# Optimization experiments

Measured on AMD Instinct MI355X. Metric: run time of the kernel, lower is better.

The kernel has to match this reference:

```python
import jax, jax.numpy as jnp
import numpy as np

N = 131072
MUL = 128                      # multiplicity of each irrep block in the input
IN_DIM = MUL * (1 + 3 + 5)     # 128x0e + 128x1o + 128x2e = 1152
INV_SQRT_MUL = 1.0 / np.sqrt(MUL)  # e3nn o3.Linear path normalization (fan_in = 128)

# --- Clebsch-Gordan (wigner 3j) tensors for 1o x 1o -> 0e, 1e, 2e ------------
# e3nn real basis ordering for l=1 is (y, z, x): index 0=y, 1=z, 2=x.

def _w3j_110():
    # 0e output: dot product; sum of squares of entries = 1
    return np.eye(3, dtype=np.float32) / np.sqrt(3.0)

def _w3j_111():
    # 1e output: Levi-Civita (cross product), normalized so sum of squares = 1
    eps = np.zeros((3, 3, 3), np.float32)
    for i, j, k in [(0, 1, 2), (1, 2, 0), (2, 0, 1)]:
        eps[i, j, k] = 1.0
        eps[j, i, k] = -1.0
    return eps / np.sqrt(6.0)

def _w3j_112():
    # 2e output: symmetric traceless rank-2 part.
    # l=2 component order: (xy, yz, 3z^2-r^2, xz, x^2-y^2); l=1 axes (y,z,x).
    Y, Z, X = 0, 1, 2
    s2 = 1.0 / np.sqrt(2.0)
    s6 = 1.0 / np.sqrt(6.0)
    M = np.zeros((3, 3, 5), np.float32)
    M[X, Y, 0] = M[Y, X, 0] = s2
    M[Y, Z, 1] = M[Z, Y, 1] = s2
    M[X, X, 2] = -s6; M[Y, Y, 2] = -s6; M[Z, Z, 2] = 2.0 * s6
    M[X, Z, 3] = M[Z, X, 3] = s2
    M[X, X, 4] = s2; M[Y, Y, 4] = -s2
    return M / np.sqrt(5.0)

_C0 = jnp.asarray(_w3j_110())
_C1 = jnp.asarray(_w3j_111())
_C2 = jnp.asarray(_w3j_112())
# path weights sqrt(dim(irrep_out)) for irrep_normalization='component',
# path_normalization='element' with fan = mul1*mul2 = 1
_PW0 = 1.0
_PW1 = float(np.sqrt(3.0))
_PW2 = float(np.sqrt(5.0))


def setup_inputs() -> dict:
    key = jax.random.key(0)
    k1, k2, k3, k4 = jax.random.split(key, 4)
    x = jax.random.normal(k1, (N, IN_DIM), jnp.float32)
    W1 = jax.random.normal(k2, (MUL, MUL), jnp.float32)   # 128x1o -> 128x1o
    W2 = jax.random.normal(k3, (MUL, 2), jnp.float32)     # 128x1o -> 2x1o
    tp_w = jax.random.normal(k4, (3,), jnp.float32)       # one weight per CG path
    return {"x": x, "W1": W1, "W2": W2, "tp_w": tp_w}


def reference(x, W1, W2, tp_w):
    n = x.shape[0]
    # o3.Linear(128x0e+128x1o+128x2e -> 128x1o): only the 1o block connects.
    x1o = x[:, MUL:MUL + 3 * MUL].reshape(n, MUL, 3)
    y = jnp.einsum('nuc,uv->nvc', x1o, W1) * INV_SQRT_MUL   # [N,128,3]
    y = jax.nn.silu(y)                                      # elementwise, as in torch
    y = jnp.einsum('nuc,uv->nvc', y, W2) * INV_SQRT_MUL     # [N,2,3] == 2x1o
    a, b = y[:, 0], y[:, 1]                                 # split y[:, :3], y[:, 3:]
    out0 = (tp_w[0] * _PW0) * jnp.einsum('ij,ni,nj->n', _C0, a, b)[:, None]  # [N,1]
    out1 = (tp_w[1] * _PW1) * jnp.einsum('ijk,ni,nj->nk', _C1, a, b)          # [N,3]
    out2 = (tp_w[2] * _PW2) * jnp.einsum('ijk,ni,nj->nk', _C2, a, b)          # [N,5]
    return jnp.concatenate([out0, out1, out2], axis=-1)     # [N,9] (0e+1e+2e)
```

## Files before the change

kernel.cpp:

```cpp
#include <hip/hip_runtime.h>
#include <hip/hip_bf16.h>

#define MULC 128
#define IN_DIM 1152
#define ROWS_PER_WG 64
#define NTHREADS 256
#define W1T_PITCH 136

typedef __attribute__((ext_vector_type(8))) short bf16x8;
typedef __attribute__((ext_vector_type(4))) float f32x4;
typedef __attribute__((ext_vector_type(4))) unsigned short u16x4;

__device__ __forceinline__ unsigned short f2bf(float f) {
    unsigned int b = __builtin_bit_cast(unsigned int, f);
    b += 0x7fffu + ((b >> 16) & 1u);
    return (unsigned short)(b >> 16);
}

#define LOADC(r0,r1,r2,r3,r4,r5, kc) {                                  \
    const float4* p_ = (const float4*)(xbase + 96 * (kc));              \
    r0 = p_[0]; r1 = p_[1]; r2 = p_[2]; r3 = p_[3]; r4 = p_[4]; r5 = p_[5]; }

#define FRAGS(F0,F1,F2, r0,r1,r2,r3,r4,r5)                                         \
    bf16x8 F0 = { (short)f2bf(r0.x), (short)f2bf(r0.w), (short)f2bf(r1.z),         \
                  (short)f2bf(r2.y), (short)f2bf(r3.x), (short)f2bf(r3.w),         \
                  (short)f2bf(r4.z), (short)f2bf(r5.y) };                          \
    bf16x8 F1 = { (short)f2bf(r0.y), (short)f2bf(r1.x), (short)f2bf(r1.w),         \
                  (short)f2bf(r2.z), (short)f2bf(r3.y), (short)f2bf(r4.x),         \
                  (short)f2bf(r4.w), (short)f2bf(r5.z) };                          \
    bf16x8 F2 = { (short)f2bf(r0.z), (short)f2bf(r1.y), (short)f2bf(r2.x),         \
                  (short)f2bf(r2.w), (short)f2bf(r3.z), (short)f2bf(r4.y),         \
                  (short)f2bf(r5.x), (short)f2bf(r5.w) };

#define MFMA_STEP(kc, F0,F1,F2)                                                     \
    _Pragma("unroll")                                                               \
    for (int nt = 0; nt < 8; ++nt) {                                                \
        bf16x8 bfr = *(const bf16x8*)&lds[(nt * 16 + li) * W1T_PITCH + (kc) * 32 + g * 8]; \
        acc[0][nt] = __builtin_amdgcn_mfma_f32_16x16x32_bf16(F0, bfr, acc[0][nt], 0, 0, 0); \
        acc[1][nt] = __builtin_amdgcn_mfma_f32_16x16x32_bf16(F1, bfr, acc[1][nt], 0, 0, 0); \
        acc[2][nt] = __builtin_amdgcn_mfma_f32_16x16x32_bf16(F2, bfr, acc[2][nt], 0, 0, 0); \
    }

__global__ __launch_bounds__(NTHREADS, 2)
void nltp_kernel(const float* __restrict__ x, const float* __restrict__ W1,
                 const float* __restrict__ W2, const float* __restrict__ tpw,
                 float* __restrict__ out)
{
    __shared__ __align__(16) unsigned short lds[128 * W1T_PITCH];
    const int t  = threadIdx.x;
    const int n0 = blockIdx.x * ROWS_PER_WG;
    const int l  = t & 63;
    const int w  = t >> 6;
    const int g  = l >> 4;
    const int li = l & 15;

    const float* xbase = x + (size_t)(n0 + 16 * w + li) * IN_DIM + MULC + 24 * g;

    float4 a0,a1,a2,a3,a4,a5, b0,b1,b2,b3,b4,b5;
    LOADC(a0,a1,a2,a3,a4,a5, 0);

    for (int it = 0; it < 16; ++it) {
        int tau = it * 256 + t;
        int v   = tau & 127;
        int u   = (tau >> 7) * 4;
        float f0 = W1[(u + 0) * MULC + v];
        float f1 = W1[(u + 1) * MULC + v];
        float f2 = W1[(u + 2) * MULC + v];
        float f3 = W1[(u + 3) * MULC + v];
        u16x4 pk = { f2bf(f0), f2bf(f1), f2bf(f2), f2bf(f3) };
        *(u16x4*)&lds[v * W1T_PITCH + u] = pk;
    }
    __syncthreads();

    f32x4 acc[3][8];
#pragma unroll
    for (int c = 0; c < 3; ++c)
#pragma unroll
        for (int nt = 0; nt < 8; ++nt)
            acc[c][nt] = (f32x4){0.f, 0.f, 0.f, 0.f};

    LOADC(b0,b1,b2,b3,b4,b5, 1);
    { FRAGS(fa0,fa1,fa2, a0,a1,a2,a3,a4,a5); MFMA_STEP(0, fa0,fa1,fa2); }
    LOADC(a0,a1,a2,a3,a4,a5, 2);
    { FRAGS(fb0,fb1,fb2, b0,b1,b2,b3,b4,b5); MFMA_STEP(1, fb0,fb1,fb2); }
    LOADC(b0,b1,b2,b3,b4,b5, 3);
    { FRAGS(fc0,fc1,fc2, a0,a1,a2,a3,a4,a5); MFMA_STEP(2, fc0,fc1,fc2); }
    { FRAGS(fd0,fd1,fd2, b0,b1,b2,b3,b4,b5); MFMA_STEP(3, fd0,fd1,fd2); }

    const float inv = 0.08838834764831845f;
    float w2a[8], w2b[8];
#pragma unroll
    for (int nt = 0; nt < 8; ++nt) {
        float2 p = *(const float2*)(W2 + 2 * (nt * 16 + li));
        w2a[nt] = p.x; w2b[nt] = p.y;
    }
    float pa[3][4], pb[3][4];
#pragma unroll
    for (int c = 0; c < 3; ++c)
#pragma unroll
        for (int rg = 0; rg < 4; ++rg) { pa[c][rg] = 0.f; pb[c][rg] = 0.f; }

#pragma unroll
    for (int c = 0; c < 3; ++c)
#pragma unroll
        for (int nt = 0; nt < 8; ++nt)
#pragma unroll
            for (int rg = 0; rg < 4; ++rg) {
                float y = acc[c][nt][rg] * inv;
                float s = y / (1.f + __expf(-y));
                pa[c][rg] += s * w2a[nt];
                pb[c][rg] += s * w2b[nt];
            }

#pragma unroll
    for (int c = 0; c < 3; ++c)
#pragma unroll
        for (int rg = 0; rg < 4; ++rg) {
            float va = pa[c][rg], vb = pb[c][rg];
            va += __shfl_xor(va, 1, 16); vb += __shfl_xor(vb, 1, 16);
            va += __shfl_xor(va, 2, 16); vb += __shfl_xor(vb, 2, 16);
            va += __shfl_xor(va, 4, 16); vb += __shfl_xor(vb, 4, 16);
            va += __shfl_xor(va, 8, 16); vb += __shfl_xor(vb, 8, 16);
            pa[c][rg] = va * inv;
            pb[c][rg] = vb * inv;
        }

    const float tw0 = tpw[0], tw1 = tpw[1], tw2 = tpw[2];
    const float k0 = tw0 * 0.5773502691896258f;
    const float k1 = tw1 * 0.7071067811865476f;
    const float s2 = 0.7071067811865476f;
    const float s6 = 0.4082482904638631f;

#pragma unroll
    for (int rg = 0; rg < 4; ++rg) {
        float a_0 = pa[0][rg], a_1 = pa[1][rg], a_2 = pa[2][rg];
        float b_0 = pb[0][rg], b_1 = pb[1][rg], b_2 = pb[2][rg];
        float o0 = k0 * (a_0 * b_0 + a_1 * b_1 + a_2 * b_2);
        float o1 = k1 * (a_1 * b_2 - a_2 * b_1);
        float o2 = k1 * (a_2 * b_0 - a_0 * b_2);
        float o3 = k1 * (a_0 * b_1 - a_1 * b_0);
        float o4 = tw2 * (s2 * (a_2 * b_0 + a_0 * b_2));
        float o5 = tw2 * (s2 * (a_0 * b_1 + a_1 * b_0));
        float o6 = tw2 * (s6 * (2.f * a_1 * b_1 - a_2 * b_2 - a_0 * b_0));
        float o7 = tw2 * (s2 * (a_2 * b_1 + a_1 * b_2));
        float o8 = tw2 * (s2 * (a_2 * b_2 - a_0 * b_0));
        float o = li == 0 ? o0 : li == 1 ? o1 : li == 2 ? o2 : li == 3 ? o3 :
                  li == 4 ? o4 : li == 5 ? o5 : li == 6 ? o6 : li == 7 ? o7 : o8;
        if (li < 9) {
            int row = n0 + 16 * w + 4 * g + rg;
            out[row * 9 + li] = o;
        }
    }
}

extern "C" void kernel_launch(void* const* d_in, const int* in_sizes, int n_in,
                              void* d_out, int out_size, void* d_ws, size_t ws_size,
                              hipStream_t stream) {
    const float* x   = (const float*)d_in[0];
    const float* W1  = (const float*)d_in[1];
    const float* W2  = (const float*)d_in[2];
    const float* tpw = (const float*)d_in[3];
    float* out = (float*)d_out;
    const int n = in_sizes[0] / IN_DIM;
    dim3 grid(n / ROWS_PER_WG);
    nltp_kernel<<<grid, NTHREADS, 0, stream>>>(x, W1, W2, tpw, out);
}
```

Baseline: 64.73 us.

## Stage x tile through swizzled LDS with contiguous row loads

```diff
diff --git a/kernel.cpp b/kernel.cpp
--- a/kernel.cpp
+++ b/kernel.cpp
@@ -5,11 +5,12 @@
 #define IN_DIM 1152
 #define ROWS_PER_WG 64
 #define NTHREADS 256
-#define W1T_PITCH 136
 
 typedef __attribute__((ext_vector_type(8))) short bf16x8;
 typedef __attribute__((ext_vector_type(4))) float f32x4;
-typedef __attribute__((ext_vector_type(4))) unsigned short u16x4;
+
+#define A_BASE 16384
+#define A_PLANE 8192
 
 __device__ __forceinline__ unsigned short f2bf(float f) {
     unsigned int b = __builtin_bit_cast(unsigned int, f);
@@ -17,36 +18,12 @@
     return (unsigned short)(b >> 16);
 }
 
-#define LOADC(r0,r1,r2,r3,r4,r5, kc) {                                  \
-    const float4* p_ = (const float4*)(xbase + 96 * (kc));              \
-    r0 = p_[0]; r1 = p_[1]; r2 = p_[2]; r3 = p_[3]; r4 = p_[4]; r5 = p_[5]; }
-
-#define FRAGS(F0,F1,F2, r0,r1,r2,r3,r4,r5)                                         \
-    bf16x8 F0 = { (short)f2bf(r0.x), (short)f2bf(r0.w), (short)f2bf(r1.z),         \
-                  (short)f2bf(r2.y), (short)f2bf(r3.x), (short)f2bf(r3.w),         \
-                  (short)f2bf(r4.z), (short)f2bf(r5.y) };                          \
-    bf16x8 F1 = { (short)f2bf(r0.y), (short)f2bf(r1.x), (short)f2bf(r1.w),         \
-                  (short)f2bf(r2.z), (short)f2bf(r3.y), (short)f2bf(r4.x),         \
-                  (short)f2bf(r4.w), (short)f2bf(r5.z) };                          \
-    bf16x8 F2 = { (short)f2bf(r0.z), (short)f2bf(r1.y), (short)f2bf(r2.x),         \
-                  (short)f2bf(r2.w), (short)f2bf(r3.z), (short)f2bf(r4.y),         \
-                  (short)f2bf(r5.x), (short)f2bf(r5.w) };
-
-#define MFMA_STEP(kc, F0,F1,F2)                                                     \
-    _Pragma("unroll")                                                               \
-    for (int nt = 0; nt < 8; ++nt) {                                                \
-        bf16x8 bfr = *(const bf16x8*)&lds[(nt * 16 + li) * W1T_PITCH + (kc) * 32 + g * 8]; \
-        acc[0][nt] = __builtin_amdgcn_mfma_f32_16x16x32_bf16(F0, bfr, acc[0][nt], 0, 0, 0); \
-        acc[1][nt] = __builtin_amdgcn_mfma_f32_16x16x32_bf16(F1, bfr, acc[1][nt], 0, 0, 0); \
-        acc[2][nt] = __builtin_amdgcn_mfma_f32_16x16x32_bf16(F2, bfr, acc[2][nt], 0, 0, 0); \
-    }
-
 __global__ __launch_bounds__(NTHREADS, 2)
 void nltp_kernel(const float* __restrict__ x, const float* __restrict__ W1,
                  const float* __restrict__ W2, const float* __restrict__ tpw,
                  float* __restrict__ out)
 {
-    __shared__ __align__(16) unsigned short lds[128 * W1T_PITCH];
+    __shared__ __align__(16) unsigned short lds[40960];
     const int t  = threadIdx.x;
     const int n0 = blockIdx.x * ROWS_PER_WG;
     const int l  = t & 63;
@@ -54,21 +31,43 @@
     const int g  = l >> 4;
     const int li = l & 15;
 
-    const float* xbase = x + (size_t)(n0 + 16 * w + li) * IN_DIM + MULC + 24 * g;
+    const int r = t >> 2;
+    const int q = t & 3;
+    const float* src = x + (size_t)(n0 + r) * IN_DIM + MULC + 96 * q;
+    float4 F[24];
+#pragma unroll
+    for (int m = 0; m < 24; ++m) F[m] = ((const float4*)src)[m];
 
-    float4 a0,a1,a2,a3,a4,a5, b0,b1,b2,b3,b4,b5;
-    LOADC(a0,a1,a2,a3,a4,a5, 0);
+#pragma unroll 4
+    for (int it = 0; it < 16; ++it) {
+        int idx = it * 256 + t;
+        int u   = idx >> 5;
+        int v4  = idx & 31;
+        float4 f = ((const float4*)W1)[idx];
+        int ug = u >> 3, ur = u & 7;
+#pragma unroll
+        for (int e = 0; e < 4; ++e) {
+            int v = 4 * v4 + e;
+            lds[v * 128 + ((ug ^ (v & 7)) << 3) + ur] =
+                f2bf(e == 0 ? f.x : e == 1 ? f.y : e == 2 ? f.z : f.w);
+        }
+    }
 
-    for (int it = 0; it < 16; ++it) {
-        int tau = it * 256 + t;
-        int v   = tau & 127;
-        int u   = (tau >> 7) * 4;
-        float f0 = W1[(u + 0) * MULC + v];
-        float f1 = W1[(u + 1) * MULC + v];
-        float f2 = W1[(u + 2) * MULC + v];
-        float f3 = W1[(u + 3) * MULC + v];
-        u16x4 pk = { f2bf(f0), f2bf(f1), f2bf(f2), f2bf(f3) };
-        *(u16x4*)&lds[v * W1T_PITCH + u] = pk;
+    {
+        const float* Ff = (const float*)F;
+        const int rh = r & 7;
+#pragma unroll
+        for (int c = 0; c < 3; ++c) {
+#pragma unroll
+            for (int j = 0; j < 4; ++j) {
+                bf16x8 v;
+#pragma unroll
+                for (int s = 0; s < 8; ++s)
+                    v[s] = (short)f2bf(Ff[24 * j + 3 * s + c]);
+                int gran = (4 * q + j) ^ rh;
+                *(bf16x8*)&lds[A_BASE + c * A_PLANE + r * 128 + (gran << 3)] = v;
+            }
+        }
     }
     __syncthreads();
 
@@ -79,13 +78,24 @@
         for (int nt = 0; nt < 8; ++nt)
             acc[c][nt] = (f32x4){0.f, 0.f, 0.f, 0.f};
 
-    LOADC(b0,b1,b2,b3,b4,b5, 1);
-    { FRAGS(fa0,fa1,fa2, a0,a1,a2,a3,a4,a5); MFMA_STEP(0, fa0,fa1,fa2); }
-    LOADC(a0,a1,a2,a3,a4,a5, 2);
-    { FRAGS(fb0,fb1,fb2, b0,b1,b2,b3,b4,b5); MFMA_STEP(1, fb0,fb1,fb2); }
-    LOADC(b0,b1,b2,b3,b4,b5, 3);
-    { FRAGS(fc0,fc1,fc2, a0,a1,a2,a3,a4,a5); MFMA_STEP(2, fc0,fc1,fc2); }
-    { FRAGS(fd0,fd1,fd2, b0,b1,b2,b3,b4,b5); MFMA_STEP(3, fd0,fd1,fd2); }
+    const int ar  = 16 * w + li;
+    const int arh = ar & 7;
+    const int lih = li & 7;
+#pragma unroll
+    for (int kc = 0; kc < 4; ++kc) {
+        const int kk = kc * 4 + g;
+        bf16x8 af[3];
+#pragma unroll
+        for (int c = 0; c < 3; ++c)
+            af[c] = *(const bf16x8*)&lds[A_BASE + c * A_PLANE + ar * 128 + ((kk ^ arh) << 3)];
+#pragma unroll
+        for (int nt = 0; nt < 8; ++nt) {
+            bf16x8 bfr = *(const bf16x8*)&lds[(nt * 16 + li) * 128 + ((kk ^ lih) << 3)];
+            acc[0][nt] = __builtin_amdgcn_mfma_f32_16x16x32_bf16(af[0], bfr, acc[0][nt], 0, 0, 0);
+            acc[1][nt] = __builtin_amdgcn_mfma_f32_16x16x32_bf16(af[1], bfr, acc[1][nt], 0, 0, 0);
+            acc[2][nt] = __builtin_amdgcn_mfma_f32_16x16x32_bf16(af[2], bfr, acc[2][nt], 0, 0, 0);
+        }
+    }
 
     const float inv = 0.08838834764831845f;
     float w2a[8], w2b[8];
```

Result: slower. 87.69 us (+35.5%).
